# Optimization experiments

Measured on AMD Instinct MI355X. Metric: run time of the kernel, lower is better.

The kernel has to match this reference:

```python
import jax, jax.numpy as jnp
import numpy as np

L = 768
Z_DIM = 128
C = 32
EPS = 1e-5


def _layer_norm(x, w, b):
    mu = jnp.mean(x, axis=-1, keepdims=True)
    var = jnp.mean(jnp.square(x - mu), axis=-1, keepdims=True)
    return (x - mu) * jax.lax.rsqrt(var + EPS) * w + b


def setup_inputs() -> dict:
    key = jax.random.key(0)
    ks = jax.random.split(key, 12)
    s_z = 1.0 / np.sqrt(Z_DIM)
    s_c = 1.0 / np.sqrt(C)
    return {
        "z": jax.random.normal(ks[0], (L, L, Z_DIM), dtype=jnp.float32),
        "norm_w": jnp.ones((Z_DIM,), jnp.float32),
        "norm_b": jnp.zeros((Z_DIM,), jnp.float32),
        "onorm_w": jnp.ones((C,), jnp.float32),
        "onorm_b": jnp.zeros((C,), jnp.float32),
        "a_w": jax.random.normal(ks[1], (C, Z_DIM), jnp.float32) * s_z,
        "a_b": jnp.zeros((C,), jnp.float32),
        "ag_w": jax.random.normal(ks[2], (C, Z_DIM), jnp.float32) * s_z,
        "ag_b": jnp.zeros((C,), jnp.float32),
        "g_w": jax.random.normal(ks[3], (Z_DIM, Z_DIM), jnp.float32) * s_z,
        "g_b": jnp.zeros((Z_DIM,), jnp.float32),
        "o_w": jax.random.normal(ks[4], (Z_DIM, C), jnp.float32) * s_c,
        "o_b": jnp.zeros((Z_DIM,), jnp.float32),
    }


def reference(z, norm_w, norm_b, onorm_w, onorm_b, a_w, a_b, ag_w, ag_b, g_w, g_b, o_w, o_b):
    zn = _layer_norm(z, norm_w, norm_b)                       # [L,L,Z]
    a = (zn @ a_w.T + a_b) * jax.nn.sigmoid(zn @ ag_w.T + ag_b)  # [L,L,C]
    # source computes b with the same (a) projections -> b == a
    o = jnp.einsum('ilc,jlc->ijc', a, a)                      # [L,L,C]
    o = _layer_norm(o, onorm_w, onorm_b)
    o = o @ o_w.T + o_b                                        # [L,L,Z]
    o = o * jax.nn.sigmoid(zn @ g_w.T + g_b)
    return o
```

## Files before the change

### kernel.cpp

```cpp
#include <hip/hip_runtime.h>
#include <math.h>


#define LDIM 768
#define LL   (768 * 768)
#define ZD   128
#define CD   32

typedef __bf16 bf16x8 __attribute__((ext_vector_type(8)));
typedef float  f32x4  __attribute__((ext_vector_type(4)));

__device__ __forceinline__ ushort f2bf(float f) {
    __bf16 h = (__bf16)f;
    return __builtin_bit_cast(ushort, h);
}
__device__ __forceinline__ float bf2f(ushort u) {
    return __builtin_bit_cast(float, ((unsigned)u) << 16);
}
__device__ __forceinline__ float sigm(float x) {
    return __builtin_amdgcn_rcpf(1.0f + __expf(-x));
}

__global__ __launch_bounds__(256) void k0_frags(
    const float* __restrict__ aw, const float* __restrict__ agw,
    const float* __restrict__ gw, const float* __restrict__ ow,
    ushort* __restrict__ afrag, ushort* __restrict__ gfrag,
    ushort* __restrict__ ofrag)
{
    const int idx = blockIdx.x * 256 + threadIdx.x;
    if (idx >= 3584) return;
    const int lane = idx & 63;
    const int fr = lane & 15, hi = lane >> 4;
    union { ushort us[8]; uint4 q; } pk;
    if (idx < 1024) {
        const int f = idx >> 6, t = f >> 2, kk = f & 3;
        const float* src = ((t < 2) ? aw : agw) + ((t & 1) * 16 + fr) * ZD + kk * 32 + hi * 8;
        #pragma unroll
        for (int j = 0; j < 8; ++j) pk.us[j] = f2bf(src[j]);
        *(uint4*)&afrag[(size_t)f * 512 + lane * 8] = pk.q;
    } else if (idx < 3072) {
        const int f = (idx - 1024) >> 6, n = f >> 2, kk = f & 3;
        const float* src = gw + (n * 16 + fr) * ZD + kk * 32 + hi * 8;
        #pragma unroll
        for (int j = 0; j < 8; ++j) pk.us[j] = f2bf(src[j]);
        *(uint4*)&gfrag[(size_t)f * 512 + lane * 8] = pk.q;
    } else {
        const int n = (idx - 3072) >> 6;
        const float* src = ow + (n * 16 + fr) * CD + hi * 8;
        #pragma unroll
        for (int j = 0; j < 8; ++j) pk.us[j] = f2bf(src[j]);
        *(uint4*)&ofrag[(size_t)n * 512 + lane * 8] = pk.q;
    }
}

__global__ __launch_bounds__(256) void k1_ln_proj(
    const float* __restrict__ z, const float* __restrict__ nw, const float* __restrict__ nb,
    const ushort* __restrict__ afrag,
    const float* __restrict__ ab, const float* __restrict__ agb,
    ushort* __restrict__ a_t, ushort* __restrict__ zn_g)
{
    __shared__ ushort znw[4][16][136];

    const int tid = threadIdx.x;
    const int lane = tid & 63, wave = tid >> 6;
    const int fr = lane & 15, hi = lane >> 4;

    bf16x8 bfr[4][4];
    {
        const ushort* wl = afrag + (size_t)lane * 8;
        #pragma unroll
        for (int t = 0; t < 4; ++t)
            #pragma unroll
            for (int kk = 0; kk < 4; ++kk)
                bfr[t][kk] = *(const bf16x8*)(wl + (size_t)(t * 4 + kk) * 512);
    }
    const float ab0 = ab[fr], ab1 = ab[16 + fr];
    const float agb0 = agb[fr], agb1 = agb[16 + fr];

    const size_t blockrow = (size_t)blockIdx.x * 256;
    const int lr = lane >> 2, seg = lane & 3;

    float4 zreg[8];
    {
        const float4* zp = (const float4*)(z + (blockrow + wave * 16 + lr) * ZD + seg * 32);
        #pragma unroll
        for (int q = 0; q < 8; ++q) zreg[q] = zp[q];
    }

    for (int c = 0; c < 4; ++c) {
        const size_t rowc = blockrow + c * 64 + wave * 16;

        {
            float v[32];
            #pragma unroll
            for (int q = 0; q < 8; ++q) {
                v[q * 4 + 0] = zreg[q].x; v[q * 4 + 1] = zreg[q].y;
                v[q * 4 + 2] = zreg[q].z; v[q * 4 + 3] = zreg[q].w;
            }
            float s = 0.f, ss = 0.f;
            #pragma unroll
            for (int e = 0; e < 32; ++e) { s += v[e]; ss += v[e] * v[e]; }
            s += __shfl_xor(s, 1); ss += __shfl_xor(ss, 1);
            s += __shfl_xor(s, 2); ss += __shfl_xor(ss, 2);
            const float mu  = s * (1.f / 128.f);
            const float var = ss * (1.f / 128.f) - mu * mu;
            const float rs  = rsqrtf(var + 1e-5f);
            union { ushort u[32]; uint4 q4[4]; } pk;
            #pragma unroll
            for (int e = 0; e < 32; ++e) {
                const int k = seg * 32 + e;
                pk.u[e] = f2bf((v[e] - mu) * rs * nw[k] + nb[k]);
            }
            #pragma unroll
            for (int q = 0; q < 4; ++q)
                *(uint4*)&znw[wave][lr][seg * 32 + q * 8] = pk.q4[q];
        }

        if (c < 3) {
            const float4* zp = (const float4*)(z + (rowc + 64 + lr - wave * 16 + wave * 16) * ZD + seg * 32);
            #pragma unroll
            for (int q = 0; q < 8; ++q) zreg[q] = zp[q];
        }

        #pragma unroll
        for (int i = 0; i < 4; ++i) {
            const int r = i * 4 + hi;
            const int c8 = fr * 8;
            *(uint4*)&zn_g[(rowc + r) * ZD + c8] = *(const uint4*)&znw[wave][r][c8];
        }

        bf16x8 af[4];
        #pragma unroll
        for (int kk = 0; kk < 4; ++kk)
            af[kk] = *(const bf16x8*)&znw[wave][fr][kk * 32 + hi * 8];

        f32x4 acc[4];
        #pragma unroll
        for (int t = 0; t < 4; ++t) acc[t] = (f32x4){0.f, 0.f, 0.f, 0.f};
        #pragma unroll
        for (int kk = 0; kk < 4; ++kk)
            #pragma unroll
            for (int t = 0; t < 4; ++t)
                acc[t] = __builtin_amdgcn_mfma_f32_16x16x32_bf16(af[kk], bfr[t][kk], acc[t], 0, 0, 0);

        {
            union { ushort u[4]; uint2 d; } pk;
            #pragma unroll
            for (int q = 0; q < 4; ++q)
                pk.u[q] = f2bf((acc[0][q] + ab0) * sigm(acc[2][q] + agb0));
            *(uint2*)&a_t[(size_t)fr * LL + rowc + hi * 4] = pk.d;
            #pragma unroll
            for (int q = 0; q < 4; ++q)
                pk.u[q] = f2bf((acc[1][q] + ab1) * sigm(acc[3][q] + agb1));
            *(uint2*)&a_t[(size_t)(16 + fr) * LL + rowc + hi * 4] = pk.d;
        }
    }
}

__global__ __launch_bounds__(256) void k2_einsum(
    const ushort* __restrict__ a_t, ushort* __restrict__ obuf16)
{
    __shared__ ushort As[2][64][32];
    __shared__ ushort Bs[2][64][32];

    const int tid = threadIdx.x;
    const int c = blockIdx.y;
    int p = blockIdx.x, bi = 0;
    while (p >= 12 - bi) { p -= 12 - bi; ++bi; }
    const int bj = bi + p;
    const int i0 = bi * 64, j0 = bj * 64;
    const ushort* base = a_t + (size_t)c * LL;

    const int srow = tid >> 2, scol = (tid & 3) * 8;
    const ushort* gA = base + (size_t)(i0 + srow) * LDIM + scol;
    const ushort* gB = base + (size_t)(j0 + srow) * LDIM + scol;

    const int wave = tid >> 6, lane = tid & 63;
    const int wi = (wave >> 1) * 32, wj = (wave & 1) * 32;
    const int fr = lane & 15, k8 = (lane >> 4) * 8;

    f32x4 acc[2][2];
    #pragma unroll
    for (int m = 0; m < 2; ++m)
        #pragma unroll
        for (int n = 0; n < 2; ++n)
            acc[m][n] = (f32x4){0.f, 0.f, 0.f, 0.f};

    auto stage = [&](int b, int kc) {
        __builtin_amdgcn_global_load_lds(
            (const uint*)(gA + kc * 32), (uint*)&As[b][srow][scol], 16, 0, 0);
        __builtin_amdgcn_global_load_lds(
            (const uint*)(gB + kc * 32), (uint*)&Bs[b][srow][scol], 16, 0, 0);
    };

    stage(0, 0);
    __syncthreads();
    for (int kc = 0; kc < 24; ++kc) {
        const int cur = kc & 1;
        if (kc + 1 < 24) stage(cur ^ 1, kc + 1);

        bf16x8 av[2], bv[2];
        #pragma unroll
        for (int m = 0; m < 2; ++m)
            av[m] = *(const bf16x8*)&As[cur][wi + m * 16 + fr][k8];
        #pragma unroll
        for (int n = 0; n < 2; ++n)
            bv[n] = *(const bf16x8*)&Bs[cur][wj + n * 16 + fr][k8];

        #pragma unroll
        for (int m = 0; m < 2; ++m)
            #pragma unroll
            for (int n = 0; n < 2; ++n)
                acc[m][n] = __builtin_amdgcn_mfma_f32_16x16x32_bf16(
                    av[m], bv[n], acc[m][n], 0, 0, 0);
        __syncthreads();
    }

    ushort* ob = obuf16 + (size_t)c * LL;
    #pragma unroll
    for (int m = 0; m < 2; ++m)
        #pragma unroll
        for (int n = 0; n < 2; ++n) {
            #pragma unroll
            for (int q = 0; q < 4; ++q) {
                const int row = i0 + wi + m * 16 + (lane >> 4) * 4 + q;
                const int col = j0 + wj + n * 16 + fr;
                ob[(size_t)row * LDIM + col] = f2bf(acc[m][n][q]);
            }
            if (bi != bj) {
                const int mrow = j0 + wj + n * 16 + fr;
                const int mcol = i0 + wi + m * 16 + (lane >> 4) * 4;
                union { ushort u[4]; uint2 d; } pk;
                #pragma unroll
                for (int q = 0; q < 4; ++q) pk.u[q] = f2bf(acc[m][n][q]);
                *(uint2*)&ob[(size_t)mrow * LDIM + mcol] = pk.d;
            }
        }
}

__global__ __launch_bounds__(256) void k3_out(
    const ushort* __restrict__ obuf16, const ushort* __restrict__ zn_g,
    const float* __restrict__ onw, const float* __restrict__ onb,
    const ushort* __restrict__ gfrag, const ushort* __restrict__ ofrag,
    const float* __restrict__ obias, const float* __restrict__ gb,
    float* __restrict__ out)
{
    __shared__ float  Ol[64][33];
    __shared__ ushort An[4][16][36];
    __shared__ ushort Zl[4][16][136];
    __shared__ float  Res[4][16][68];

    const int tid = threadIdx.x;
    const int lane = tid & 63, wave = tid >> 6;
    const int fr = lane & 15, hi = lane >> 4;
    const size_t rowbase = (size_t)blockIdx.x * 64;
    const int wrow = wave * 16;

    #pragma unroll
    for (int cc = 0; cc < 4; ++cc) {
        const int ch = wave * 8 + cc * 2 + (lane >> 5);
        const int r2 = (lane & 31) * 2;
        const uint u = *(const uint*)&obuf16[(size_t)ch * LL + rowbase + r2];
        Ol[r2][ch]     = bf2f((ushort)(u & 0xffff));
        Ol[r2 + 1][ch] = bf2f((ushort)(u >> 16));
    }
    #pragma unroll
    for (int i = 0; i < 4; ++i) {
        const int r = i * 4 + hi;
        *(uint4*)&Zl[wave][r][fr * 8] =
            *(const uint4*)&zn_g[(rowbase + wrow + r) * ZD + fr * 8];
    }
    __syncthreads();

    {
        const int r = lane >> 2, seg = lane & 3;
        float v[8];
        #pragma unroll
        for (int e = 0; e < 8; ++e) v[e] = Ol[wrow + r][seg * 8 + e];
        float s = 0.f, ss = 0.f;
        #pragma unroll
        for (int e = 0; e < 8; ++e) { s += v[e]; ss += v[e] * v[e]; }
        s += __shfl_xor(s, 1); ss += __shfl_xor(ss, 1);
        s += __shfl_xor(s, 2); ss += __shfl_xor(ss, 2);
        const float mu  = s * (1.f / 32.f);
        const float var = ss * (1.f / 32.f) - mu * mu;
        const float rs  = rsqrtf(var + 1e-5f);
        union { ushort us[8]; uint4 q; } pk;
        #pragma unroll
        for (int e = 0; e < 8; ++e) {
            const int c = seg * 8 + e;
            pk.us[e] = f2bf((v[e] - mu) * rs * onw[c] + onb[c]);
        }
        *(uint4*)&An[wave][r][seg * 8] = pk.q;
    }

    const bf16x8 afo = *(const bf16x8*)&An[wave][fr][hi * 8];
    bf16x8 afg[4];
    #pragma unroll
    for (int kk = 0; kk < 4; ++kk)
        afg[kk] = *(const bf16x8*)&Zl[wave][fr][kk * 32 + hi * 8];

    const ushort* gl = gfrag + (size_t)lane * 8;
    const ushort* ol = ofrag + (size_t)lane * 8;
    f32x4 po[8], pg[8];
    #pragma unroll
    for (int n = 0; n < 8; ++n) {
        po[n] = __builtin_amdgcn_mfma_f32_16x16x32_bf16(
            afo, *(const bf16x8*)(ol + (size_t)n * 512),
            (f32x4){0.f, 0.f, 0.f, 0.f}, 0, 0, 0);
        pg[n] = (f32x4){0.f, 0.f, 0.f, 0.f};
        #pragma unroll
        for (int kk = 0; kk < 4; ++kk)
            pg[n] = __builtin_amdgcn_mfma_f32_16x16x32_bf16(
                afg[kk], *(const bf16x8*)(gl + (size_t)(n * 4 + kk) * 512),
                pg[n], 0, 0, 0);
    }

    #pragma unroll
    for (int h = 0; h < 2; ++h) {
        #pragma unroll
        for (int nn = 0; nn < 4; ++nn) {
            const int n = h * 4 + nn;
            const int ch = n * 16 + fr;
            const float obv = obias[ch], gbv = gb[ch];
            #pragma unroll
            for (int q = 0; q < 4; ++q)
                Res[wave][hi * 4 + q][nn * 16 + fr] =
                    (po[n][q] + obv) * sigm(pg[n][q] + gbv);
        }
        #pragma unroll
        for (int i = 0; i < 4; ++i) {
            const int r = i * 4 + hi;
            *(float4*)&out[(rowbase + wrow + r) * ZD + h * 64 + fr * 4] =
                *(const float4*)&Res[wave][r][fr * 4];
        }
    }
}

extern "C" void kernel_launch(void* const* d_in, const int* in_sizes, int n_in,
                              void* d_out, int out_size, void* d_ws, size_t ws_size,
                              hipStream_t stream) {
    (void)in_sizes; (void)n_in; (void)out_size; (void)ws_size;
    const float* z   = (const float*)d_in[0];
    const float* nw  = (const float*)d_in[1];
    const float* nb  = (const float*)d_in[2];
    const float* onw = (const float*)d_in[3];
    const float* onb = (const float*)d_in[4];
    const float* aw  = (const float*)d_in[5];
    const float* ab  = (const float*)d_in[6];
    const float* agw = (const float*)d_in[7];
    const float* agb = (const float*)d_in[8];
    const float* gw  = (const float*)d_in[9];
    const float* gb  = (const float*)d_in[10];
    const float* ow  = (const float*)d_in[11];
    const float* ob  = (const float*)d_in[12];

    char* ws = (char*)d_ws;
    ushort* a_t    = (ushort*)ws;
    ushort* zn_g   = (ushort*)(ws + 37748736);
    ushort* obuf16 = (ushort*)(ws + 188743680);
    ushort* afrag  = (ushort*)(ws + 226492416);
    ushort* gfrag  = (ushort*)(ws + 226508800);
    ushort* ofrag  = (ushort*)(ws + 226541568);

    k0_frags<<<14, 256, 0, stream>>>(aw, agw, gw, ow, afrag, gfrag, ofrag);
    k1_ln_proj<<<LL / 256, 256, 0, stream>>>(z, nw, nb, afrag, ab, agb,
                                             a_t, zn_g);
    k2_einsum<<<dim3(78, 32), 256, 0, stream>>>(a_t, obuf16);
    k3_out<<<LL / 64, 256, 0, stream>>>(obuf16, zn_g, onw, onb, gfrag, ofrag,
                                        ob, gb, (float*)d_out);
}
```

Measured before the change: 312.2 us.

## Store normalized z in MFMA fragment layout and drop k3 LDS staging

k1 now writes the bf16 normalized z directly in MFMA A-fragment order, so k3 can load its operand fragments straight from global memory into registers. This removes k3's Zl and An shared-memory buffers and the LDS round trip, and the output-norm fragment is now built with cross-lane shuffles. The projection loop is split into two halves to lower register pressure, and Res padding changes to 69. The goal is less LDS traffic and better occupancy in k3, at the cost of a scattered store pattern in k1.

```diff
diff --git a/kernel.cpp b/kernel.cpp
--- a/kernel.cpp
+++ b/kernel.cpp
@@ -57,7 +57,7 @@
     const float* __restrict__ z, const float* __restrict__ nw, const float* __restrict__ nb,
     const ushort* __restrict__ afrag,
     const float* __restrict__ ab, const float* __restrict__ agb,
-    ushort* __restrict__ a_t, ushort* __restrict__ zn_g)
+    ushort* __restrict__ a_t, ushort* __restrict__ znfrag)
 {
     __shared__ ushort znw[4][16][136];
 
@@ -89,7 +89,9 @@
 
     for (int c = 0; c < 4; ++c) {
         const size_t rowc = blockrow + c * 64 + wave * 16;
-
+        const size_t tile = rowc >> 4;
+
+        union { ushort u[32]; uint4 q4[4]; } pk;
         {
             float v[32];
             #pragma unroll
@@ -105,28 +107,23 @@
             const float mu  = s * (1.f / 128.f);
             const float var = ss * (1.f / 128.f) - mu * mu;
             const float rs  = rsqrtf(var + 1e-5f);
-            union { ushort u[32]; uint4 q4[4]; } pk;
             #pragma unroll
             for (int e = 0; e < 32; ++e) {
                 const int k = seg * 32 + e;
                 pk.u[e] = f2bf((v[e] - mu) * rs * nw[k] + nb[k]);
             }
-            #pragma unroll
-            for (int q = 0; q < 4; ++q)
-                *(uint4*)&znw[wave][lr][seg * 32 + q * 8] = pk.q4[q];
-        }
+        }
+        #pragma unroll
+        for (int q = 0; q < 4; ++q)
+            *(uint4*)&znw[wave][lr][seg * 32 + q * 8] = pk.q4[q];
+        #pragma unroll
+        for (int h2 = 0; h2 < 4; ++h2)
+            *(uint4*)&znfrag[((tile * 4 + seg) * 64 + lr + 16 * h2) * 8] = pk.q4[h2];
 
         if (c < 3) {
-            const float4* zp = (const float4*)(z + (rowc + 64 + lr - wave * 16 + wave * 16) * ZD + seg * 32);
+            const float4* zp = (const float4*)(z + (rowc + 64 + lr) * ZD + seg * 32);
             #pragma unroll
             for (int q = 0; q < 8; ++q) zreg[q] = zp[q];
-        }
-
-        #pragma unroll
-        for (int i = 0; i < 4; ++i) {
-            const int r = i * 4 + hi;
-            const int c8 = fr * 8;
-            *(uint4*)&zn_g[(rowc + r) * ZD + c8] = *(const uint4*)&znw[wave][r][c8];
         }
 
         bf16x8 af[4];
@@ -144,15 +141,15 @@
                 acc[t] = __builtin_amdgcn_mfma_f32_16x16x32_bf16(af[kk], bfr[t][kk], acc[t], 0, 0, 0);
 
         {
-            union { ushort u[4]; uint2 d; } pk;
+            union { ushort u[4]; uint2 d; } pw;
             #pragma unroll
             for (int q = 0; q < 4; ++q)
-                pk.u[q] = f2bf((acc[0][q] + ab0) * sigm(acc[2][q] + agb0));
-            *(uint2*)&a_t[(size_t)fr * LL + rowc + hi * 4] = pk.d;
+                pw.u[q] = f2bf((acc[0][q] + ab0) * sigm(acc[2][q] + agb0));
+            *(uint2*)&a_t[(size_t)fr * LL + rowc + hi * 4] = pw.d;
             #pragma unroll
             for (int q = 0; q < 4; ++q)
-                pk.u[q] = f2bf((acc[1][q] + ab1) * sigm(acc[3][q] + agb1));
-            *(uint2*)&a_t[(size_t)(16 + fr) * LL + rowc + hi * 4] = pk.d;
+                pw.u[q] = f2bf((acc[1][q] + ab1) * sigm(acc[3][q] + agb1));
+            *(uint2*)&a_t[(size_t)(16 + fr) * LL + rowc + hi * 4] = pw.d;
         }
     }
 }
@@ -239,22 +236,26 @@
 }
 
 __global__ __launch_bounds__(256) void k3_out(
-    const ushort* __restrict__ obuf16, const ushort* __restrict__ zn_g,
+    const ushort* __restrict__ obuf16, const ushort* __restrict__ znfrag,
     const float* __restrict__ onw, const float* __restrict__ onb,
     const ushort* __restrict__ gfrag, const ushort* __restrict__ ofrag,
     const float* __restrict__ obias, const float* __restrict__ gb,
     float* __restrict__ out)
 {
-    __shared__ float  Ol[64][33];
-    __shared__ ushort An[4][16][36];
-    __shared__ ushort Zl[4][16][136];
-    __shared__ float  Res[4][16][68];
+    __shared__ float Ol[64][33];
+    __shared__ float Res[4][16][69];
 
     const int tid = threadIdx.x;
     const int lane = tid & 63, wave = tid >> 6;
     const int fr = lane & 15, hi = lane >> 4;
     const size_t rowbase = (size_t)blockIdx.x * 64;
     const int wrow = wave * 16;
+    const size_t tile = (rowbase + wrow) >> 4;
+
+    bf16x8 afg[4];
+    #pragma unroll
+    for (int kk = 0; kk < 4; ++kk)
+        afg[kk] = *(const bf16x8*)&znfrag[((tile * 4 + kk) * 64 + lane) * 8];
 
     #pragma unroll
     for (int cc = 0; cc < 4; ++cc) {
@@ -264,14 +265,9 @@
         Ol[r2][ch]     = bf2f((ushort)(u & 0xffff));
         Ol[r2 + 1][ch] = bf2f((ushort)(u >> 16));
     }
-    #pragma unroll
-    for (int i = 0; i < 4; ++i) {
-        const int r = i * 4 + hi;
-        *(uint4*)&Zl[wave][r][fr * 8] =
-            *(const uint4*)&zn_g[(rowbase + wrow + r) * ZD + fr * 8];
-    }
     __syncthreads();
 
+    union { ushort us[8]; uint u4[4]; } anp;
     {
         const int r = lane >> 2, seg = lane & 3;
         float v[8];
@@ -285,48 +281,49 @@
         const float mu  = s * (1.f / 32.f);
         const float var = ss * (1.f / 32.f) - mu * mu;
         const float rs  = rsqrtf(var + 1e-5f);
-        union { ushort us[8]; uint4 q; } pk;
         #pragma unroll
         for (int e = 0; e < 8; ++e) {
             const int c = seg * 8 + e;
-            pk.us[e] = f2bf((v[e] - mu) * rs * onw[c] + onb[c]);
-        }
-        *(uint4*)&An[wave][r][seg * 8] = pk.q;
-    }
-
-    const bf16x8 afo = *(const bf16x8*)&An[wave][fr][hi * 8];
-    bf16x8 afg[4];
-    #pragma unroll
-    for (int kk = 0; kk < 4; ++kk)
-        afg[kk] = *(const bf16x8*)&Zl[wave][fr][kk * 32 + hi * 8];
-
-    const ushort* gl = gfrag + (size_t)lane * 8;
-    const ushort* ol = ofrag + (size_t)lane * 8;
-    f32x4 po[8], pg[8];
-    #pragma unroll
-    for (int n = 0; n < 8; ++n) {
-        po[n] = __builtin_amdgcn_mfma_f32_16x16x32_bf16(
-            afo, *(const bf16x8*)(ol + (size_t)n * 512),
-            (f32x4){0.f, 0.f, 0.f, 0.f}, 0, 0, 0);
-        pg[n] = (f32x4){0.f, 0.f, 0.f, 0.f};
-        #pragma unroll
-        for (int kk = 0; kk < 4; ++kk)
-            pg[n] = __builtin_amdgcn_mfma_f32_16x16x32_bf16(
-                afg[kk], *(const bf16x8*)(gl + (size_t)(n * 4 + kk) * 512),
-                pg[n], 0, 0, 0);
-    }
+            anp.us[e] = f2bf((v[e] - mu) * rs * onw[c] + onb[c]);
+        }
+    }
+    bf16x8 afo;
+    {
+        const int src = 4 * fr + hi;
+        union { uint u[4]; bf16x8 v; } t;
+        #pragma unroll
+        for (int m = 0; m < 4; ++m)
+            t.u[m] = (uint)__shfl((int)anp.u4[m], src);
+        afo = t.v;
+    }
+
+    const ushort* glp = gfrag + (size_t)lane * 8;
+    const ushort* olp = ofrag + (size_t)lane * 8;
 
     #pragma unroll
     for (int h = 0; h < 2; ++h) {
+        f32x4 po[4], pg[4];
         #pragma unroll
         for (int nn = 0; nn < 4; ++nn) {
             const int n = h * 4 + nn;
-            const int ch = n * 16 + fr;
+            po[nn] = __builtin_amdgcn_mfma_f32_16x16x32_bf16(
+                afo, *(const bf16x8*)(olp + (size_t)n * 512),
+                (f32x4){0.f, 0.f, 0.f, 0.f}, 0, 0, 0);
+            pg[nn] = (f32x4){0.f, 0.f, 0.f, 0.f};
+            #pragma unroll
+            for (int kk = 0; kk < 4; ++kk)
+                pg[nn] = __builtin_amdgcn_mfma_f32_16x16x32_bf16(
+                    afg[kk], *(const bf16x8*)(glp + (size_t)(n * 4 + kk) * 512),
+                    pg[nn], 0, 0, 0);
+        }
+        #pragma unroll
+        for (int nn = 0; nn < 4; ++nn) {
+            const int ch = (h * 4 + nn) * 16 + fr;
             const float obv = obias[ch], gbv = gb[ch];
             #pragma unroll
             for (int q = 0; q < 4; ++q)
                 Res[wave][hi * 4 + q][nn * 16 + fr] =
-                    (po[n][q] + obv) * sigm(pg[n][q] + gbv);
+                    (po[nn][q] + obv) * sigm(pg[nn][q] + gbv);
         }
         #pragma unroll
         for (int i = 0; i < 4; ++i) {
@@ -357,7 +354,7 @@
 
     char* ws = (char*)d_ws;
     ushort* a_t    = (ushort*)ws;
-    ushort* zn_g   = (ushort*)(ws + 37748736);
+    ushort* znfrag = (ushort*)(ws + 37748736);
     ushort* obuf16 = (ushort*)(ws + 188743680);
     ushort* afrag  = (ushort*)(ws + 226492416);
     ushort* gfrag  = (ushort*)(ws + 226508800);
@@ -365,8 +362,8 @@
 
     k0_frags<<<14, 256, 0, stream>>>(aw, agw, gw, ow, afrag, gfrag, ofrag);
     k1_ln_proj<<<LL / 256, 256, 0, stream>>>(z, nw, nb, afrag, ab, agb,
-                                             a_t, zn_g);
+                                             a_t, znfrag);
     k2_einsum<<<dim3(78, 32), 256, 0, stream>>>(a_t, obuf16);
-    k3_out<<<LL / 64, 256, 0, stream>>>(obuf16, zn_g, onw, onb, gfrag, ofrag,
+    k3_out<<<LL / 64, 256, 0, stream>>>(obuf16, znfrag, onw, onb, gfrag, ofrag,
                                         ob, gb, (float*)d_out);
 }
```

Result: slower. 318.8 us (+2.1%).
